# Optimization experiments

Measured on AMD Instinct MI355X. Metric: run time of the kernel, lower is better.

## Reference

```python
import jax, jax.numpy as jnp
import numpy as np

B, S, E, H, FF = 4, 1024, 1024, 16, 4096
D = E // H
EPS = 1e-5


def layer_norm(x, g, b):
    m = jnp.mean(x, axis=-1, keepdims=True)
    v = jnp.var(x, axis=-1, keepdims=True)
    return (x - m) / jnp.sqrt(v + EPS) * g + b


def setup_inputs() -> dict:
    key = jax.random.key(0)
    ks = jax.random.split(key, 12)
    x = jax.random.normal(ks[0], (B, S, E), dtype=jnp.float32)
    # binary attention mask [B,S,S]; force diagonal=1 so no row is fully masked
    mask = jax.random.randint(ks[1], (B, S, S), 0, 2).astype(jnp.float32)
    idx = jnp.arange(S)
    mask = mask.at[:, idx, idx].set(1.0)
    gnn_adj = jax.random.normal(ks[2], (B, S, S), dtype=jnp.float32) * 0.02
    sc = 0.02
    params = dict(
        Wq=jax.random.normal(ks[3], (E, E), dtype=jnp.float32) * sc, bq=jnp.zeros((E,), jnp.float32),
        Wk=jax.random.normal(ks[4], (E, E), dtype=jnp.float32) * sc, bk=jnp.zeros((E,), jnp.float32),
        Wv=jax.random.normal(ks[5], (E, E), dtype=jnp.float32) * sc, bv=jnp.zeros((E,), jnp.float32),
        Wo=jax.random.normal(ks[6], (E, E), dtype=jnp.float32) * sc, bo=jnp.zeros((E,), jnp.float32),
        g1=jnp.ones((E,), jnp.float32), b1=jnp.zeros((E,), jnp.float32),
        g2=jnp.ones((E,), jnp.float32), b2=jnp.zeros((E,), jnp.float32),
        W1=jax.random.normal(ks[7], (E, FF), dtype=jnp.float32) * sc, bf1=jnp.zeros((FF,), jnp.float32),
        W2=jax.random.normal(ks[8], (FF, E), dtype=jnp.float32) * sc, bf2=jnp.zeros((E,), jnp.float32),
    )
    return dict(x=x, mask=mask, gnn_adj=gnn_adj, **params)


def reference(x, mask, gnn_adj, Wq, bq, Wk, bk, Wv, bv, Wo, bo, g1, b1, g2, b2, W1, bf1, W2, bf2):
    # pre-norm (norm_first=True), dropout = identity (eval)
    nx = layer_norm(x, g1, b1)
    # QKV projections -> [B,H,S,D]
    def split_heads(t):
        return t.reshape(B, S, H, D).transpose(0, 2, 1, 3)
    q = split_heads(nx @ Wq + bq)
    k = split_heads(nx @ Wk + bk)
    v = split_heads(nx @ Wv + bv)
    scores = jnp.einsum('bhqd,bhkd->bhqk', q, k) / jnp.sqrt(jnp.float32(D))
    m = mask[:, None]  # [B,1,S,S]
    scores = jnp.where(m == 0, -jnp.inf, scores * m)
    attn = jax.nn.softmax(scores, axis=-1)
    # non-standard: additive bias AFTER softmax
    attn = attn + gnn_adj[:, None]
    xv = jnp.einsum('bhqk,bhkd->bhqd', attn, v)
    xv = xv.transpose(0, 2, 1, 3).reshape(B, S, E)
    x = x + (xv @ Wo + bo)
    h = layer_norm(x, g2, b2)
    ff = jax.nn.gelu(h @ W1 + bf1, approximate=False) @ W2 + bf2
    return x + ff
```

## Files before the change

### kernel.cpp

```cpp
#include <hip/hip_runtime.h>
#include <hip/hip_bf16.h>

typedef unsigned short u16;
typedef short bf16x8 __attribute__((ext_vector_type(8)));
typedef float f32x4 __attribute__((ext_vector_type(4)));

#define B_ 4
#define S_ 1024
#define E_ 1024
#define H_ 16
#define FF_ 4096
#define D_ 64
#define M_ 4096

__device__ __forceinline__ u16 f2bf(float f) {
  unsigned int u = __builtin_bit_cast(unsigned int, f);
  u += 0x7fffu + ((u >> 16) & 1u);
  return (u16)(u >> 16);
}
__device__ __forceinline__ float bf2f(u16 v) {
  unsigned int u = ((unsigned int)v) << 16;
  return __builtin_bit_cast(float, u);
}

__device__ __forceinline__ void gld_lds16(const void* g, void* l) {
  __builtin_amdgcn_global_load_lds((__attribute__((address_space(1))) void*)g,
                                   (__attribute__((address_space(3))) void*)l,
                                   16, 0, 0);
}

__global__ void __launch_bounds__(256) cast_transpose_all(
    const float* __restrict__ wq, const float* __restrict__ wk,
    const float* __restrict__ wv, const float* __restrict__ wo,
    const float* __restrict__ w1, const float* __restrict__ w2,
    u16* __restrict__ wt) {
  int bid = blockIdx.x;
  const float* src; u16* dst; int K, N; int local;
  if (bid < 4096) {
    int wsel = bid >> 10; local = bid & 1023; K = 1024; N = 1024;
    src = wsel == 0 ? wq : wsel == 1 ? wk : wsel == 2 ? wv : wo;
    dst = wt + (size_t)wsel * 1024 * 1024;
  } else if (bid < 8192) {
    local = bid - 4096; K = 1024; N = 4096; src = w1;
    dst = wt + (size_t)4 * 1024 * 1024;
  } else {
    local = bid - 8192; K = 4096; N = 1024; src = w2;
    dst = wt + (size_t)8 * 1024 * 1024;
  }
  int tiles_n = N >> 5;
  int n0 = (local % tiles_n) << 5, k0 = (local / tiles_n) << 5;
  __shared__ float tl[32][33];
  int tx = threadIdx.x & 31, ty = threadIdx.x >> 5;
#pragma unroll
  for (int i = 0; i < 4; ++i)
    tl[ty + i * 8][tx] = src[(size_t)(k0 + ty + i * 8) * N + n0 + tx];
  __syncthreads();
#pragma unroll
  for (int i = 0; i < 4; ++i)
    dst[(size_t)(n0 + ty + i * 8) * K + k0 + tx] = f2bf(tl[tx][ty + i * 8]);
}

__global__ void __launch_bounds__(256) cast_maskgnn(
    const float* __restrict__ mask, const float* __restrict__ gnn,
    u16* __restrict__ biasI, u16* __restrict__ gnnbf) {
  int row = blockIdx.x;
  int b = row >> 10, q = row & 1023;
  int t = threadIdx.x;
  __shared__ float mrow[1024];
  const float* mp = mask + ((size_t)row << 10);
  const float* gp = gnn + ((size_t)row << 10);
  float4 mv = *(const float4*)(mp + t * 4);
  *(float4*)(mrow + t * 4) = mv;
  float4 gv = *(const float4*)(gp + t * 4);
  ushort4 g4;
  g4.x = f2bf(gv.x); g4.y = f2bf(gv.y); g4.z = f2bf(gv.z); g4.w = f2bf(gv.w);
  *(ushort4*)(gnnbf + ((size_t)row << 10) + t * 4) = g4;
  __syncthreads();
  int kt = t >> 4, c = t & 15;
  const u16 NEG = f2bf(-30008.f);
  const u16 SHIFT = f2bf(-8.0f);
  ushort4 o;
  o.x = (mrow[kt * 64 + c] == 0.f) ? NEG : SHIFT;
  o.y = (mrow[kt * 64 + 16 + c] == 0.f) ? NEG : SHIFT;
  o.z = (mrow[kt * 64 + 32 + c] == 0.f) ? NEG : SHIFT;
  o.w = (mrow[kt * 64 + 48 + c] == 0.f) ? NEG : SHIFT;
  *(ushort4*)(biasI + (((size_t)(b * 16 + kt) << 10) + q) * 64 + c * 4) = o;
}

__global__ void __launch_bounds__(256) vtrans_kernel(
    const u16* __restrict__ v, u16* __restrict__ vt) {
  int st = blockIdx.x, h = blockIdx.y, b = blockIdx.z;
  __shared__ u16 tl[64][72];
  const u16* src = v + ((((size_t)(b * 16 + h)) << 10) + (st << 6)) * 64;
  int r = threadIdx.x >> 2, g = (threadIdx.x & 3) << 4;
  *(uint4*)&tl[r][g] = *(const uint4*)(src + r * 64 + g);
  *(uint4*)&tl[r][g + 8] = *(const uint4*)(src + r * 64 + g + 8);
  __syncthreads();
  u16 tmp[16];
#pragma unroll
  for (int i = 0; i < 16; ++i) tmp[i] = tl[g + i][r];
  u16* dst = vt + ((size_t)b << 20) + (((size_t)(h * 64 + r)) << 10) + (st << 6) + g;
  *(uint4*)(dst) = *(uint4*)(tmp);
  *(uint4*)(dst + 8) = *(uint4*)(tmp + 8);
}

__global__ void __launch_bounds__(256) ln_kernel(
    const float* __restrict__ x, const float* __restrict__ g,
    const float* __restrict__ bt, u16* __restrict__ out) {
  int row = blockIdx.x, t = threadIdx.x;
  const float* xr = x + (size_t)row * 1024;
  float4 v = *(const float4*)(xr + t * 4);
  float s = v.x + v.y + v.z + v.w;
  float q = v.x * v.x + v.y * v.y + v.z * v.z + v.w * v.w;
#pragma unroll
  for (int off = 1; off < 64; off <<= 1) {
    s += __shfl_xor(s, off);
    q += __shfl_xor(q, off);
  }
  __shared__ float sb[4], qb[4];
  int w = t >> 6, l = t & 63;
  if (l == 0) { sb[w] = s; qb[w] = q; }
  __syncthreads();
  s = sb[0] + sb[1] + sb[2] + sb[3];
  q = qb[0] + qb[1] + qb[2] + qb[3];
  float mean = s * (1.f / 1024.f);
  float var = q * (1.f / 1024.f) - mean * mean;
  float rs = rsqrtf(var + 1e-5f);
  float4 gv = *(const float4*)(g + t * 4);
  float4 bv = *(const float4*)(bt + t * 4);
  ushort4 o;
  o.x = f2bf((v.x - mean) * rs * gv.x + bv.x);
  o.y = f2bf((v.y - mean) * rs * gv.y + bv.y);
  o.z = f2bf((v.z - mean) * rs * gv.z + bv.z);
  o.w = f2bf((v.w - mean) * rs * gv.w + bv.w);
  *(ushort4*)(out + (size_t)row * 1024 + t * 4) = o;
}

__device__ __forceinline__ void gemm_core_db(
    const u16* __restrict__ A, int lda, const u16* __restrict__ Bt, int ldb,
    int nkt, int bm, int bn, u16* lds, f32x4 acc[4][4]) {
  const int tid = threadIdx.x;
  const int w = tid >> 6, l = tid & 63;
  const int wm = (w >> 1) << 6, wn = (w & 1) << 6;
  const int lrow = l >> 3;
  const int cg = (l & 7) ^ lrow;
  const u16* Ab = A + (size_t)(bm << 7) * lda;
  const u16* Bb = Bt + (size_t)(bn << 7) * ldb;
#define GSTAGE(T, BUF)                                                       \
  {                                                                          \
    int kk = (T) << 6;                                                       \
    u16* la = lds + (BUF) * 16384;                                           \
    u16* lb = la + 8192;                                                     \
    _Pragma("unroll") for (int i = 0; i < 4; ++i) {                          \
      int c = (w << 2) + i;                                                  \
      int row = (c << 3) + lrow;                                             \
      gld_lds16(Ab + (size_t)row * lda + kk + (cg << 3), la + (c << 9));     \
      gld_lds16(Bb + (size_t)row * ldb + kk + (cg << 3), lb + (c << 9));     \
    }                                                                        \
  }
  GSTAGE(0, 0);
  __syncthreads();
  for (int t = 0; t < nkt; ++t) {
    if (t + 1 < nkt) GSTAGE(t + 1, (t & 1) ^ 1);
    const u16* la = lds + (t & 1) * 16384;
    const u16* lb = la + 8192;
    bf16x8 af[2][4], bfr[2][4];
    const int rr = l & 15;
    const int kgb = l >> 4;
#pragma unroll
    for (int ks = 0; ks < 2; ++ks) {
      const int kg = kgb + (ks << 2);
#pragma unroll
      for (int f = 0; f < 4; ++f) {
        int ra = wm + (f << 4) + rr;
        af[ks][f] = *(const bf16x8*)(la + (ra << 6) + ((kg ^ (ra & 7)) << 3));
        int rb = wn + (f << 4) + rr;
        bfr[ks][f] = *(const bf16x8*)(lb + (rb << 6) + ((kg ^ (rb & 7)) << 3));
      }
    }
#pragma unroll
    for (int fm = 0; fm < 4; ++fm)
#pragma unroll
      for (int fn = 0; fn < 4; ++fn)
#pragma unroll
        for (int ks = 0; ks < 2; ++ks)
          acc[fm][fn] = __builtin_amdgcn_mfma_f32_16x16x32_bf16(
              af[ks][fm], bfr[ks][fn], acc[fm][fn], 0, 0, 0);
    __syncthreads();
  }
#undef GSTAGE
}

__device__ __forceinline__ void gemm_core_db64(
    const u16* __restrict__ A, int lda, const u16* __restrict__ Bt, int ldb,
    int nkt, int bm, int bn, u16* lds, f32x4 acc[4][2]) {
  const int tid = threadIdx.x;
  const int w = tid >> 6, l = tid & 63;
  const int wn = w << 5;
  const int lrow = l >> 3;
  const int cg = (l & 7) ^ lrow;
  const u16* Ab = A + (size_t)(bm << 6) * lda;
  const u16* Bb = Bt + (size_t)(bn << 7) * ldb;
#define GSTAGE64(T, BUF)                                                     \
  {                                                                          \
    int kk = (T) << 6;                                                       \
    u16* la = lds + (BUF) * 12288;                                           \
    u16* lb = la + 4096;                                                     \
    _Pragma("unroll") for (int i = 0; i < 2; ++i) {                          \
      int c = (w << 1) + i;                                                  \
      int row = (c << 3) + lrow;                                             \
      gld_lds16(Ab + (size_t)row * lda + kk + (cg << 3), la + (c << 9));     \
    }                                                                        \
    _Pragma("unroll") for (int i = 0; i < 4; ++i) {                          \
      int c = (w << 2) + i;                                                  \
      int row = (c << 3) + lrow;                                             \
      gld_lds16(Bb + (size_t)row * ldb + kk + (cg << 3), lb + (c << 9));     \
    }                                                                        \
  }
  GSTAGE64(0, 0);
  __syncthreads();
  for (int t = 0; t < nkt; ++t) {
    if (t + 1 < nkt) GSTAGE64(t + 1, (t & 1) ^ 1);
    const u16* la = lds + (t & 1) * 12288;
    const u16* lb = la + 4096;
    bf16x8 af[2][4], bfr[2][2];
    const int rr = l & 15;
    const int kgb = l >> 4;
#pragma unroll
    for (int ks = 0; ks < 2; ++ks) {
      const int kg = kgb + (ks << 2);
#pragma unroll
      for (int f = 0; f < 4; ++f) {
        int ra = (f << 4) + rr;
        af[ks][f] = *(const bf16x8*)(la + (ra << 6) + ((kg ^ (ra & 7)) << 3));
      }
#pragma unroll
      for (int f = 0; f < 2; ++f) {
        int rb = wn + (f << 4) + rr;
        bfr[ks][f] = *(const bf16x8*)(lb + (rb << 6) + ((kg ^ (rb & 7)) << 3));
      }
    }
#pragma unroll
    for (int fm = 0; fm < 4; ++fm)
#pragma unroll
      for (int fn = 0; fn < 2; ++fn)
#pragma unroll
        for (int ks = 0; ks < 2; ++ks)
          acc[fm][fn] = __builtin_amdgcn_mfma_f32_16x16x32_bf16(
              af[ks][fm], bfr[ks][fn], acc[fm][fn], 0, 0, 0);
    __syncthreads();
  }
#undef GSTAGE64
}

#define ACC_INIT()                        \
  f32x4 acc[4][4];                        \
  { f32x4 zf = {0.f, 0.f, 0.f, 0.f};      \
_Pragma("unroll")                         \
    for (int a = 0; a < 4; ++a)           \
_Pragma("unroll")                         \
      for (int bb = 0; bb < 4; ++bb) acc[a][bb] = zf; }

#define ACC_INIT64()                      \
  f32x4 acc[4][2];                        \
  { f32x4 zf = {0.f, 0.f, 0.f, 0.f};      \
_Pragma("unroll")                         \
    for (int a = 0; a < 4; ++a)           \
_Pragma("unroll")                         \
      for (int bb = 0; bb < 2; ++bb) acc[a][bb] = zf; }

#define EPI_SETUP()                                     \
  const int w = threadIdx.x >> 6, l = threadIdx.x & 63; \
  const int wm = (w >> 1) << 6, wn = (w & 1) << 6;

#define EPI_SETUP64()                                   \
  const int w = threadIdx.x >> 6, l = threadIdx.x & 63; \
  const int wn = w << 5;

#define GEMM_LDS()   __shared__ __attribute__((aligned(16))) u16 lds[2 * 2 * 8192]
#define GEMM_LDS64() __shared__ __attribute__((aligned(16))) u16 lds[2 * 12288]

__global__ void __launch_bounds__(256, 2) gemm_qkv(
    const u16* __restrict__ nx, const u16* __restrict__ wt,
    const float* __restrict__ bq, const float* __restrict__ bk,
    const float* __restrict__ bv, u16* __restrict__ qk, u16* __restrict__ vtmp) {
  GEMM_LDS();
  ACC_INIT();
  int z = blockIdx.z;
  const u16* Bt = wt + (size_t)z * 1024 * 1024;
  const float* bias = z == 0 ? bq : z == 1 ? bk : bv;
  u16* out = z == 2 ? vtmp : qk + (size_t)z * M_ * 1024;
  const float scl = (z == 0) ? 0.18033688f : 1.0f;
  gemm_core_db(nx, 1024, Bt, 1024, 16, blockIdx.x, blockIdx.y, lds, acc);
  EPI_SETUP();
#pragma unroll
  for (int fm = 0; fm < 4; ++fm)
#pragma unroll
    for (int fn = 0; fn < 4; ++fn)
#pragma unroll
      for (int j = 0; j < 4; ++j) {
        int row = (blockIdx.x << 7) + wm + (fm << 4) + ((l >> 4) << 2) + j;
        int col = (blockIdx.y << 7) + wn + (fn << 4) + (l & 15);
        float v = (acc[fm][fn][j] + bias[col]) * scl;
        int b = row >> 10, s = row & 1023;
        int h = col >> 6, d = col & 63;
        out[(((size_t)(b * 16 + h) << 10) + s) * 64 + d] = f2bf(v);
      }
}

__global__ void __launch_bounds__(256, 2) gemm_gnnv(
    const u16* __restrict__ gnnbf, const u16* __restrict__ vt,
    u16* __restrict__ xvg) {
  GEMM_LDS64();
  ACC_INIT64();
  int b = blockIdx.z;
  const u16* A = gnnbf + ((size_t)b << 20);
  const u16* Bt = vt + ((size_t)b << 20);
  u16* out = xvg + ((size_t)b << 20);
  gemm_core_db64(A, 1024, Bt, 1024, 16, blockIdx.x, blockIdx.y, lds, acc);
  EPI_SETUP64();
#pragma unroll
  for (int fm = 0; fm < 4; ++fm)
#pragma unroll
    for (int fn = 0; fn < 2; ++fn)
#pragma unroll
      for (int j = 0; j < 4; ++j) {
        int row = (blockIdx.x << 6) + (fm << 4) + ((l >> 4) << 2) + j;
        int col = (blockIdx.y << 7) + wn + (fn << 4) + (l & 15);
        out[((size_t)row << 10) + col] = f2bf(acc[fm][fn][j]);
      }
}

__global__ void __launch_bounds__(256, 2) gemm_wo(
    const u16* __restrict__ xv, const u16* __restrict__ wt,
    const float* __restrict__ bo, const float* __restrict__ xres,
    float* __restrict__ x1) {
  GEMM_LDS64();
  ACC_INIT64();
  gemm_core_db64(xv, 1024, wt, 1024, 16, blockIdx.x, blockIdx.y, lds, acc);
  EPI_SETUP64();
#pragma unroll
  for (int fm = 0; fm < 4; ++fm)
#pragma unroll
    for (int fn = 0; fn < 2; ++fn)
#pragma unroll
      for (int j = 0; j < 4; ++j) {
        int row = (blockIdx.x << 6) + (fm << 4) + ((l >> 4) << 2) + j;
        int col = (blockIdx.y << 7) + wn + (fn << 4) + (l & 15);
        size_t idx = ((size_t)row << 10) + col;
        x1[idx] = acc[fm][fn][j] + bo[col] + xres[idx];
      }
}

__global__ void __launch_bounds__(256, 2) gemm_w1(
    const u16* __restrict__ hb, const u16* __restrict__ wt,
    const float* __restrict__ bf1, u16* __restrict__ ff1) {
  GEMM_LDS();
  ACC_INIT();
  gemm_core_db(hb, 1024, wt, 1024, 16, blockIdx.x, blockIdx.y, lds, acc);
  EPI_SETUP();
#pragma unroll
  for (int fm = 0; fm < 4; ++fm)
#pragma unroll
    for (int fn = 0; fn < 4; ++fn)
#pragma unroll
      for (int j = 0; j < 4; ++j) {
        int row = (blockIdx.x << 7) + wm + (fm << 4) + ((l >> 4) << 2) + j;
        int col = (blockIdx.y << 7) + wn + (fn << 4) + (l & 15);
        float v = acc[fm][fn][j] + bf1[col];
        float ge = 0.5f * v * (1.f + erff(v * 0.70710678118654752f));
        ff1[((size_t)row << 12) + col] = f2bf(ge);
      }
}

__global__ void __launch_bounds__(256, 2) gemm_w2(
    const u16* __restrict__ ff1, const u16* __restrict__ wt,
    const float* __restrict__ bf2, const float* __restrict__ x1,
    float* __restrict__ out) {
  GEMM_LDS64();
  ACC_INIT64();
  gemm_core_db64(ff1, 4096, wt, 4096, 64, blockIdx.x, blockIdx.y, lds, acc);
  EPI_SETUP64();
#pragma unroll
  for (int fm = 0; fm < 4; ++fm)
#pragma unroll
    for (int fn = 0; fn < 2; ++fn)
#pragma unroll
      for (int j = 0; j < 4; ++j) {
        int row = (blockIdx.x << 6) + (fm << 4) + ((l >> 4) << 2) + j;
        int col = (blockIdx.y << 7) + wn + (fn << 4) + (l & 15);
        size_t idx = ((size_t)row << 10) + col;
        out[idx] = acc[fm][fn][j] + bf2[col] + x1[idx];
      }
}

__global__ void __launch_bounds__(256, 2) attn_kernel(
    const u16* __restrict__ Q, const u16* __restrict__ K,
    const u16* __restrict__ Vt, const u16* __restrict__ biasI,
    const u16* __restrict__ xvg, u16* __restrict__ xv) {
  const int lin = ((blockIdx.x & 7) << 6) + (blockIdx.x >> 3);
  const int qt = lin & 7, h = (lin >> 3) & 15, b = lin >> 7;
  const int tid = threadIdx.x, w = tid >> 6, l = tid & 63;
  __shared__ __attribute__((aligned(16))) u16 kbuf[2][64 * 64];
  __shared__ __attribute__((aligned(16))) u16 vbuf[2][64 * 64];
  __shared__ __attribute__((aligned(16))) u16 pbuf[4][32 * 64];
  const size_t bh = ((size_t)(b * 16 + h)) << 16;
  const u16* Qb = Q + bh;
  const u16* Kb = K + bh;
  const u16* Vtb = Vt + ((size_t)b << 20) + ((size_t)(h * 64) << 10);
  const u16* biasb = biasI + ((size_t)b << 20);
  const int q0 = (qt << 7) + (w << 5);
  const int lrow = l >> 3, cg = (l & 7) ^ lrow;
  const int l4 = l >> 4, lo = l & 15;
  u16* p_w = pbuf[w];

  bf16x8 qf[2][2];
#pragma unroll
  for (int m = 0; m < 2; ++m)
#pragma unroll
    for (int ks = 0; ks < 2; ++ks)
      qf[m][ks] = *(const bf16x8*)(Qb + ((size_t)(q0 + m * 16 + lo) << 6) +
                                   l4 * 8 + ks * 32);
  bf16x8 onesf;
#pragma unroll
  for (int j = 0; j < 8; ++j) onesf[j] = (short)0x3F80;

  f32x4 osoft[2][4], osum[2];
  f32x4 zf = {0.f, 0.f, 0.f, 0.f};
#pragma unroll
  for (int m = 0; m < 2; ++m) {
    osum[m] = zf;
#pragma unroll
    for (int fd = 0; fd < 4; ++fd) osoft[m][fd] = zf;
  }

#define STAGE(T, BUF)                                                          \
  {                                                                            \
    int kv0s = (T) << 6;                                                       \
    u16* kd = &kbuf[BUF][0];                                                   \
    u16* vd = &vbuf[BUF][0];                                                   \
    _Pragma("unroll") for (int i = 0; i < 2; ++i) {                            \
      int c = (w << 1) + i;                                                    \
      gld_lds16(Kb + ((size_t)(kv0s + (c << 3) + lrow) << 6) + (cg << 3),      \
                kd + (c << 9));                                                \
      gld_lds16(Vtb + ((size_t)((c << 3) + lrow) << 10) + kv0s + (cg << 3),    \
                vd + (c << 9));                                                \
    }                                                                          \
  }

  STAGE(0, 0);
  __syncthreads();

  for (int t = 0; t < 16; ++t) {
    const int cur = t & 1;
    if (t < 15) STAGE(t + 1, cur ^ 1);
    const u16* kb_ = &kbuf[cur][0];
    const u16* vb_ = &vbuf[cur][0];
    f32x4 sacc[2][4];
#pragma unroll
    for (int m = 0; m < 2; ++m)
#pragma unroll
      for (int j = 0; j < 4; ++j) {
        ushort4 bb = *(const ushort4*)(
            biasb + (((size_t)(t * 1024 + q0 + m * 16 + l4 * 4 + j)) << 6) +
            lo * 4);
        sacc[m][0][j] = bf2f(bb.x);
        sacc[m][1][j] = bf2f(bb.y);
        sacc[m][2][j] = bf2f(bb.z);
        sacc[m][3][j] = bf2f(bb.w);
      }
    __builtin_amdgcn_s_setprio(1);
#pragma unroll
    for (int ks = 0; ks < 2; ++ks) {
      const int kg = l4 + (ks << 2);
      bf16x8 kf[4];
#pragma unroll
      for (int fn = 0; fn < 4; ++fn) {
        int rk = (fn << 4) + lo;
        kf[fn] = *(const bf16x8*)(kb_ + (rk << 6) + ((kg ^ (rk & 7)) << 3));
      }
#pragma unroll
      for (int m = 0; m < 2; ++m)
#pragma unroll
        for (int fn = 0; fn < 4; ++fn)
          sacc[m][fn] = __builtin_amdgcn_mfma_f32_16x16x32_bf16(
              qf[m][ks], kf[fn], sacc[m][fn], 0, 0, 0);
    }
    __builtin_amdgcn_s_setprio(0);
#pragma unroll
    for (int m = 0; m < 2; ++m)
#pragma unroll
      for (int fn = 0; fn < 4; ++fn)
#pragma unroll
        for (int j = 0; j < 4; ++j) {
          float p = exp2f(sacc[m][fn][j]);
          unsigned int u = __builtin_bit_cast(unsigned int, p);
          int prow = (m << 4) + (l4 << 2) + j;
          int pcol = (fn << 4) + lo;
          p_w[(prow << 6) + (pcol ^ ((prow & 7) << 3))] =
              (u16)((u + 0x8000u) >> 16);
        }
    __builtin_amdgcn_s_setprio(1);
#pragma unroll
    for (int ks = 0; ks < 2; ++ks) {
      const int kg = l4 + (ks << 2);
      bf16x8 pf[2], vf[4];
#pragma unroll
      for (int m = 0; m < 2; ++m) {
        int pr = (m << 4) + lo;
        pf[m] = *(const bf16x8*)(p_w + (pr << 6) + ((kg ^ (pr & 7)) << 3));
      }
#pragma unroll
      for (int fd = 0; fd < 4; ++fd) {
        int rd = (fd << 4) + lo;
        vf[fd] = *(const bf16x8*)(vb_ + (rd << 6) + ((kg ^ (rd & 7)) << 3));
      }
#pragma unroll
      for (int m = 0; m < 2; ++m) {
        osum[m] = __builtin_amdgcn_mfma_f32_16x16x32_bf16(
            pf[m], onesf, osum[m], 0, 0, 0);
#pragma unroll
        for (int fd = 0; fd < 4; ++fd)
          osoft[m][fd] = __builtin_amdgcn_mfma_f32_16x16x32_bf16(
              pf[m], vf[fd], osoft[m][fd], 0, 0, 0);
      }
    }
    __builtin_amdgcn_s_setprio(0);
    __syncthreads();
  }
#pragma unroll
  for (int m = 0; m < 2; ++m) {
    f32x4 rl;
#pragma unroll
    for (int j = 0; j < 4; ++j) rl[j] = 1.0f / osum[m][j];
#pragma unroll
    for (int fd = 0; fd < 4; ++fd)
#pragma unroll
      for (int j = 0; j < 4; ++j) {
        int qrow = q0 + (m << 4) + (l4 << 2) + j;
        int e = (h << 6) + (fd << 4) + lo;
        size_t idx = (((size_t)(b * 1024 + qrow)) << 10) + e;
        float o = osoft[m][fd][j] * rl[j] + bf2f(xvg[idx]);
        xv[idx] = f2bf(o);
      }
  }
#undef STAGE
}

extern "C" void kernel_launch(void* const* d_in, const int* in_sizes, int n_in,
                              void* d_out, int out_size, void* d_ws, size_t ws_size,
                              hipStream_t stream) {
  (void)in_sizes; (void)n_in; (void)out_size; (void)ws_size;
  const float* x   = (const float*)d_in[0];
  const float* mask= (const float*)d_in[1];
  const float* gnn = (const float*)d_in[2];
  const float* Wq  = (const float*)d_in[3];
  const float* bq  = (const float*)d_in[4];
  const float* Wk  = (const float*)d_in[5];
  const float* bk  = (const float*)d_in[6];
  const float* Wv  = (const float*)d_in[7];
  const float* bv  = (const float*)d_in[8];
  const float* Wo  = (const float*)d_in[9];
  const float* bo  = (const float*)d_in[10];
  const float* g1  = (const float*)d_in[11];
  const float* b1  = (const float*)d_in[12];
  const float* g2  = (const float*)d_in[13];
  const float* b2  = (const float*)d_in[14];
  const float* W1  = (const float*)d_in[15];
  const float* bf1 = (const float*)d_in[16];
  const float* W2  = (const float*)d_in[17];
  const float* bf2 = (const float*)d_in[18];
  float* out = (float*)d_out;

  char* ws = (char*)d_ws;
  const size_t MB = 1024 * 1024;
  u16*  wt    = (u16*)(ws);
  u16*  nx    = (u16*)(ws + 24 * MB);
  u16*  xvbuf = (u16*)(ws + 24 * MB);
  u16*  hbuf  = (u16*)(ws + 24 * MB);
  u16*  qk    = (u16*)(ws + 32 * MB);
  u16*  vt    = (u16*)(ws + 48 * MB);
  u16*  biasI = (u16*)(ws + 56 * MB);
  u16*  gnnbf = (u16*)(ws + 64 * MB);
  u16*  vtmp  = (u16*)(ws + 72 * MB);
  u16*  xvg   = (u16*)(ws + 72 * MB);
  float* x1   = (float*)(ws + 64 * MB);
  u16*  ff1   = (u16*)(ws + 32 * MB);

  cast_transpose_all<<<12288, 256, 0, stream>>>(Wq, Wk, Wv, Wo, W1, W2, wt);
  ln_kernel<<<4096, 256, 0, stream>>>(x, g1, b1, nx);
  cast_maskgnn<<<4096, 256, 0, stream>>>(mask, gnn, biasI, gnnbf);
  gemm_qkv<<<dim3(32, 8, 3), 256, 0, stream>>>(nx, wt, bq, bk, bv, qk, vtmp);
  vtrans_kernel<<<dim3(16, 16, 4), 256, 0, stream>>>(vtmp, vt);
  gemm_gnnv<<<dim3(16, 8, 4), 256, 0, stream>>>(gnnbf, vt, xvg);
  attn_kernel<<<512, 256, 0, stream>>>(
      qk, qk + (size_t)4 * MB, vt, biasI, xvg, xvbuf);
  gemm_wo<<<dim3(64, 8), 256, 0, stream>>>(xvbuf, wt + (size_t)3 * MB, bo, x, x1);
  ln_kernel<<<4096, 256, 0, stream>>>(x1, g2, b2, hbuf);
  gemm_w1<<<dim3(32, 32), 256, 0, stream>>>(hbuf, wt + (size_t)4 * MB, bf1, ff1);
  gemm_w2<<<dim3(64, 8), 256, 0, stream>>>(ff1, wt + (size_t)8 * MB, bf2, x1, out);
}
```

Baseline: 233.6 us.

## Use 64-row GEMM tiles for QKV/W1 and store residual x1 as bf16

The QKV and W1 projections switch from the 128x128 GEMM core to the 64x128 core, doubling the grid so more blocks are resident and each block holds fewer accumulators. The intermediate residual x1 is now stored in bf16 instead of fp32, with a new LayerNorm kernel that reads bf16 input, which halves that buffer's traffic. In exchange, the smaller tiles reuse each loaded tile less, and rounding the residual to bf16 loses precision in the final output.

```diff
diff --git a/kernel.cpp b/kernel.cpp
--- a/kernel.cpp
+++ b/kernel.cpp
@@ -136,59 +136,37 @@
   *(ushort4*)(out + (size_t)row * 1024 + t * 4) = o;
 }
 
-__device__ __forceinline__ void gemm_core_db(
-    const u16* __restrict__ A, int lda, const u16* __restrict__ Bt, int ldb,
-    int nkt, int bm, int bn, u16* lds, f32x4 acc[4][4]) {
-  const int tid = threadIdx.x;
-  const int w = tid >> 6, l = tid & 63;
-  const int wm = (w >> 1) << 6, wn = (w & 1) << 6;
-  const int lrow = l >> 3;
-  const int cg = (l & 7) ^ lrow;
-  const u16* Ab = A + (size_t)(bm << 7) * lda;
-  const u16* Bb = Bt + (size_t)(bn << 7) * ldb;
-#define GSTAGE(T, BUF)                                                       \
-  {                                                                          \
-    int kk = (T) << 6;                                                       \
-    u16* la = lds + (BUF) * 16384;                                           \
-    u16* lb = la + 8192;                                                     \
-    _Pragma("unroll") for (int i = 0; i < 4; ++i) {                          \
-      int c = (w << 2) + i;                                                  \
-      int row = (c << 3) + lrow;                                             \
-      gld_lds16(Ab + (size_t)row * lda + kk + (cg << 3), la + (c << 9));     \
-      gld_lds16(Bb + (size_t)row * ldb + kk + (cg << 3), lb + (c << 9));     \
-    }                                                                        \
-  }
-  GSTAGE(0, 0);
-  __syncthreads();
-  for (int t = 0; t < nkt; ++t) {
-    if (t + 1 < nkt) GSTAGE(t + 1, (t & 1) ^ 1);
-    const u16* la = lds + (t & 1) * 16384;
-    const u16* lb = la + 8192;
-    bf16x8 af[2][4], bfr[2][4];
-    const int rr = l & 15;
-    const int kgb = l >> 4;
-#pragma unroll
-    for (int ks = 0; ks < 2; ++ks) {
-      const int kg = kgb + (ks << 2);
-#pragma unroll
-      for (int f = 0; f < 4; ++f) {
-        int ra = wm + (f << 4) + rr;
-        af[ks][f] = *(const bf16x8*)(la + (ra << 6) + ((kg ^ (ra & 7)) << 3));
-        int rb = wn + (f << 4) + rr;
-        bfr[ks][f] = *(const bf16x8*)(lb + (rb << 6) + ((kg ^ (rb & 7)) << 3));
-      }
-    }
-#pragma unroll
-    for (int fm = 0; fm < 4; ++fm)
-#pragma unroll
-      for (int fn = 0; fn < 4; ++fn)
-#pragma unroll
-        for (int ks = 0; ks < 2; ++ks)
-          acc[fm][fn] = __builtin_amdgcn_mfma_f32_16x16x32_bf16(
-              af[ks][fm], bfr[ks][fn], acc[fm][fn], 0, 0, 0);
-    __syncthreads();
-  }
-#undef GSTAGE
+__global__ void __launch_bounds__(256) ln_kernel_b(
+    const u16* __restrict__ x, const float* __restrict__ g,
+    const float* __restrict__ bt, u16* __restrict__ out) {
+  int row = blockIdx.x, t = threadIdx.x;
+  const u16* xr = x + ((size_t)row << 10);
+  ushort4 xv4 = *(const ushort4*)(xr + t * 4);
+  float v0 = bf2f(xv4.x), v1 = bf2f(xv4.y), v2 = bf2f(xv4.z), v3 = bf2f(xv4.w);
+  float s = v0 + v1 + v2 + v3;
+  float q = v0 * v0 + v1 * v1 + v2 * v2 + v3 * v3;
+#pragma unroll
+  for (int off = 1; off < 64; off <<= 1) {
+    s += __shfl_xor(s, off);
+    q += __shfl_xor(q, off);
+  }
+  __shared__ float sb[4], qb[4];
+  int w = t >> 6, l = t & 63;
+  if (l == 0) { sb[w] = s; qb[w] = q; }
+  __syncthreads();
+  s = sb[0] + sb[1] + sb[2] + sb[3];
+  q = qb[0] + qb[1] + qb[2] + qb[3];
+  float mean = s * (1.f / 1024.f);
+  float var = q * (1.f / 1024.f) - mean * mean;
+  float rs = rsqrtf(var + 1e-5f);
+  float4 gv = *(const float4*)(g + t * 4);
+  float4 bv = *(const float4*)(bt + t * 4);
+  ushort4 o;
+  o.x = f2bf((v0 - mean) * rs * gv.x + bv.x);
+  o.y = f2bf((v1 - mean) * rs * gv.y + bv.y);
+  o.z = f2bf((v2 - mean) * rs * gv.z + bv.z);
+  o.w = f2bf((v3 - mean) * rs * gv.w + bv.w);
+  *(ushort4*)(out + ((size_t)row << 10) + t * 4) = o;
 }
 
 __device__ __forceinline__ void gemm_core_db64(
@@ -253,14 +231,6 @@
 #undef GSTAGE64
 }
 
-#define ACC_INIT()                        \
-  f32x4 acc[4][4];                        \
-  { f32x4 zf = {0.f, 0.f, 0.f, 0.f};      \
-_Pragma("unroll")                         \
-    for (int a = 0; a < 4; ++a)           \
-_Pragma("unroll")                         \
-      for (int bb = 0; bb < 4; ++bb) acc[a][bb] = zf; }
-
 #define ACC_INIT64()                      \
   f32x4 acc[4][2];                        \
   { f32x4 zf = {0.f, 0.f, 0.f, 0.f};      \
@@ -269,37 +239,32 @@
 _Pragma("unroll")                         \
       for (int bb = 0; bb < 2; ++bb) acc[a][bb] = zf; }
 
-#define EPI_SETUP()                                     \
-  const int w = threadIdx.x >> 6, l = threadIdx.x & 63; \
-  const int wm = (w >> 1) << 6, wn = (w & 1) << 6;
-
 #define EPI_SETUP64()                                   \
   const int w = threadIdx.x >> 6, l = threadIdx.x & 63; \
   const int wn = w << 5;
 
-#define GEMM_LDS()   __shared__ __attribute__((aligned(16))) u16 lds[2 * 2 * 8192]
 #define GEMM_LDS64() __shared__ __attribute__((aligned(16))) u16 lds[2 * 12288]
 
 __global__ void __launch_bounds__(256, 2) gemm_qkv(
     const u16* __restrict__ nx, const u16* __restrict__ wt,
     const float* __restrict__ bq, const float* __restrict__ bk,
     const float* __restrict__ bv, u16* __restrict__ qk, u16* __restrict__ vtmp) {
-  GEMM_LDS();
-  ACC_INIT();
+  GEMM_LDS64();
+  ACC_INIT64();
   int z = blockIdx.z;
   const u16* Bt = wt + (size_t)z * 1024 * 1024;
   const float* bias = z == 0 ? bq : z == 1 ? bk : bv;
   u16* out = z == 2 ? vtmp : qk + (size_t)z * M_ * 1024;
   const float scl = (z == 0) ? 0.18033688f : 1.0f;
-  gemm_core_db(nx, 1024, Bt, 1024, 16, blockIdx.x, blockIdx.y, lds, acc);
-  EPI_SETUP();
+  gemm_core_db64(nx, 1024, Bt, 1024, 16, blockIdx.x, blockIdx.y, lds, acc);
+  EPI_SETUP64();
 #pragma unroll
   for (int fm = 0; fm < 4; ++fm)
 #pragma unroll
-    for (int fn = 0; fn < 4; ++fn)
-#pragma unroll
-      for (int j = 0; j < 4; ++j) {
-        int row = (blockIdx.x << 7) + wm + (fm << 4) + ((l >> 4) << 2) + j;
+    for (int fn = 0; fn < 2; ++fn)
+#pragma unroll
+      for (int j = 0; j < 4; ++j) {
+        int row = (blockIdx.x << 6) + (fm << 4) + ((l >> 4) << 2) + j;
         int col = (blockIdx.y << 7) + wn + (fn << 4) + (l & 15);
         float v = (acc[fm][fn][j] + bias[col]) * scl;
         int b = row >> 10, s = row & 1023;
@@ -334,7 +299,7 @@
 __global__ void __launch_bounds__(256, 2) gemm_wo(
     const u16* __restrict__ xv, const u16* __restrict__ wt,
     const float* __restrict__ bo, const float* __restrict__ xres,
-    float* __restrict__ x1) {
+    u16* __restrict__ x1b) {
   GEMM_LDS64();
   ACC_INIT64();
   gemm_core_db64(xv, 1024, wt, 1024, 16, blockIdx.x, blockIdx.y, lds, acc);
@@ -348,24 +313,24 @@
         int row = (blockIdx.x << 6) + (fm << 4) + ((l >> 4) << 2) + j;
         int col = (blockIdx.y << 7) + wn + (fn << 4) + (l & 15);
         size_t idx = ((size_t)row << 10) + col;
-        x1[idx] = acc[fm][fn][j] + bo[col] + xres[idx];
+        x1b[idx] = f2bf(acc[fm][fn][j] + bo[col] + xres[idx]);
       }
 }
 
 __global__ void __launch_bounds__(256, 2) gemm_w1(
     const u16* __restrict__ hb, const u16* __restrict__ wt,
     const float* __restrict__ bf1, u16* __restrict__ ff1) {
-  GEMM_LDS();
-  ACC_INIT();
-  gemm_core_db(hb, 1024, wt, 1024, 16, blockIdx.x, blockIdx.y, lds, acc);
-  EPI_SETUP();
+  GEMM_LDS64();
+  ACC_INIT64();
+  gemm_core_db64(hb, 1024, wt, 1024, 16, blockIdx.x, blockIdx.y, lds, acc);
+  EPI_SETUP64();
 #pragma unroll
   for (int fm = 0; fm < 4; ++fm)
 #pragma unroll
-    for (int fn = 0; fn < 4; ++fn)
-#pragma unroll
-      for (int j = 0; j < 4; ++j) {
-        int row = (blockIdx.x << 7) + wm + (fm << 4) + ((l >> 4) << 2) + j;
+    for (int fn = 0; fn < 2; ++fn)
+#pragma unroll
+      for (int j = 0; j < 4; ++j) {
+        int row = (blockIdx.x << 6) + (fm << 4) + ((l >> 4) << 2) + j;
         int col = (blockIdx.y << 7) + wn + (fn << 4) + (l & 15);
         float v = acc[fm][fn][j] + bf1[col];
         float ge = 0.5f * v * (1.f + erff(v * 0.70710678118654752f));
@@ -375,7 +340,7 @@
 
 __global__ void __launch_bounds__(256, 2) gemm_w2(
     const u16* __restrict__ ff1, const u16* __restrict__ wt,
-    const float* __restrict__ bf2, const float* __restrict__ x1,
+    const float* __restrict__ bf2, const u16* __restrict__ x1b,
     float* __restrict__ out) {
   GEMM_LDS64();
   ACC_INIT64();
@@ -390,7 +355,7 @@
         int row = (blockIdx.x << 6) + (fm << 4) + ((l >> 4) << 2) + j;
         int col = (blockIdx.y << 7) + wn + (fn << 4) + (l & 15);
         size_t idx = ((size_t)row << 10) + col;
-        out[idx] = acc[fm][fn][j] + bf2[col] + x1[idx];
+        out[idx] = acc[fm][fn][j] + bf2[col] + bf2f(x1b[idx]);
       }
 }
 
@@ -582,21 +547,21 @@
   u16*  vt    = (u16*)(ws + 48 * MB);
   u16*  biasI = (u16*)(ws + 56 * MB);
   u16*  gnnbf = (u16*)(ws + 64 * MB);
+  u16*  x1b   = (u16*)(ws + 64 * MB);
   u16*  vtmp  = (u16*)(ws + 72 * MB);
   u16*  xvg   = (u16*)(ws + 72 * MB);
-  float* x1   = (float*)(ws + 64 * MB);
   u16*  ff1   = (u16*)(ws + 32 * MB);
 
   cast_transpose_all<<<12288, 256, 0, stream>>>(Wq, Wk, Wv, Wo, W1, W2, wt);
   ln_kernel<<<4096, 256, 0, stream>>>(x, g1, b1, nx);
   cast_maskgnn<<<4096, 256, 0, stream>>>(mask, gnn, biasI, gnnbf);
-  gemm_qkv<<<dim3(32, 8, 3), 256, 0, stream>>>(nx, wt, bq, bk, bv, qk, vtmp);
+  gemm_qkv<<<dim3(64, 8, 3), 256, 0, stream>>>(nx, wt, bq, bk, bv, qk, vtmp);
   vtrans_kernel<<<dim3(16, 16, 4), 256, 0, stream>>>(vtmp, vt);
   gemm_gnnv<<<dim3(16, 8, 4), 256, 0, stream>>>(gnnbf, vt, xvg);
   attn_kernel<<<512, 256, 0, stream>>>(
       qk, qk + (size_t)4 * MB, vt, biasI, xvg, xvbuf);
-  gemm_wo<<<dim3(64, 8), 256, 0, stream>>>(xvbuf, wt + (size_t)3 * MB, bo, x, x1);
-  ln_kernel<<<4096, 256, 0, stream>>>(x1, g2, b2, hbuf);
-  gemm_w1<<<dim3(32, 32), 256, 0, stream>>>(hbuf, wt + (size_t)4 * MB, bf1, ff1);
-  gemm_w2<<<dim3(64, 8), 256, 0, stream>>>(ff1, wt + (size_t)8 * MB, bf2, x1, out);
-}
+  gemm_wo<<<dim3(64, 8), 256, 0, stream>>>(xvbuf, wt + (size_t)3 * MB, bo, x, x1b);
+  ln_kernel_b<<<4096, 256, 0, stream>>>(x1b, g2, b2, hbuf);
+  gemm_w1<<<dim3(64, 32), 256, 0, stream>>>(hbuf, wt + (size_t)4 * MB, bf1, ff1);
+  gemm_w2<<<dim3(64, 8), 256, 0, stream>>>(ff1, wt + (size_t)8 * MB, bf2, x1b, out);
+}
```

Result: no change. 233.0 us (-0.3%).
